# Performance work log

Measured on AMD Instinct MI355X. Metric: run time of the kernel, lower is better.

Reference implementation:

```python
import jax, jax.numpy as jnp
import numpy as np

L, H, HM, E = 2, 1024, 256, 64  # layers, hidden, hyper hidden, hyper embedding
B, T, D = 64, 256, 1024         # batch, time, input size (D == H so layers stack)


def setup_inputs() -> dict:
    key = jax.random.key(0)
    ks = jax.random.split(key, 16)
    n = jax.random.normal
    inp = {
        'x':   n(ks[0], (B, T, D), jnp.float32),
        # main LSTM weights: 4 gates (i,f,g,o); last dim is the input dim
        'Wx':  n(ks[1], (L, 4, H, D), jnp.float32) / np.sqrt(D),
        'Wh':  n(ks[2], (L, 4, H, H), jnp.float32) / np.sqrt(H),
        # hyper (meta) LSTM: input is concat(x_t, h) of size D+H
        'Wmx': n(ks[3], (L, 4 * HM, D + H), jnp.float32) / np.sqrt(D + H),
        'Wmh': n(ks[4], (L, 4 * HM, HM), jnp.float32) / np.sqrt(HM),
        'bm':  jnp.zeros((L, 4 * HM), jnp.float32),
        # hyper embeddings z per gate (hidden->4xE projections)
        'Wzx': n(ks[5], (L, HM, 4, E), jnp.float32) / np.sqrt(HM),
        'bzx': jnp.ones((L, 4, E), jnp.float32),
        'Wzh': n(ks[6], (L, HM, 4, E), jnp.float32) / np.sqrt(HM),
        'bzh': jnp.ones((L, 4, E), jnp.float32),
        'Wzb': n(ks[7], (L, HM, 4, E), jnp.float32) / np.sqrt(HM),
        # embedding -> per-unit modulation (E->H per gate)
        'Px':  n(ks[8], (L, 4, E, H), jnp.float32) / np.sqrt(E),
        'Ph':  n(ks[9], (L, 4, E, H), jnp.float32) / np.sqrt(E),
        'Pb':  n(ks[10], (L, 4, E, H), jnp.float32) / np.sqrt(E),
    }
    return inp


def _meta_lstm_forward(x, Wx, Wh, Wmx, Wmh, bm, Wzx, bzx, Wzh, bzh, Wzb, Px, Ph, Pb):
    Bb = x.shape[0]
    inp = x
    for l in range(L):
        def step(carry, xt, l=l):
            h, c, mh, mc = carry
            # hyper LSTM step on concat(x_t, h)
            xcat = jnp.concatenate([xt, h], axis=-1)
            mpre = xcat @ Wmx[l].T + mh @ Wmh[l].T + bm[l]
            mi, mf, mg, mo = jnp.split(mpre, 4, axis=-1)
            mc2 = jax.nn.sigmoid(mf) * mc + jax.nn.sigmoid(mi) * jnp.tanh(mg)
            mh2 = jax.nn.sigmoid(mo) * jnp.tanh(mc2)
            # gate embeddings and per-unit modulation vectors [B,4,H]
            zx = jnp.einsum('bm,mge->bge', mh2, Wzx[l]) + bzx[l]
            zh = jnp.einsum('bm,mge->bge', mh2, Wzh[l]) + bzh[l]
            zb = jnp.einsum('bm,mge->bge', mh2, Wzb[l])
            dx = jnp.einsum('bge,geh->bgh', zx, Px[l])
            dh = jnp.einsum('bge,geh->bgh', zh, Ph[l])
            db = jnp.einsum('bge,geh->bgh', zb, Pb[l])
            # main LSTM gate pre-activations, hyper-modulated
            gx = jnp.einsum('bd,ghd->bgh', xt, Wx[l])
            gh = jnp.einsum('bk,ghk->bgh', h, Wh[l])
            pre = dx * gx + dh * gh + db
            i_, f_, g_, o_ = pre[:, 0], pre[:, 1], pre[:, 2], pre[:, 3]
            c2 = jax.nn.sigmoid(f_) * c + jax.nn.sigmoid(i_) * jnp.tanh(g_)
            h2 = jax.nn.sigmoid(o_) * jnp.tanh(c2)
            return (h2, c2, mh2, mc2), h2
        init = (jnp.zeros((Bb, H), x.dtype), jnp.zeros((Bb, H), x.dtype),
                jnp.zeros((Bb, HM), x.dtype), jnp.zeros((Bb, HM), x.dtype))
        xs = jnp.swapaxes(inp, 0, 1)  # [T,B,D]
        _, hs = jax.lax.scan(step, init, xs)
        inp = jnp.swapaxes(hs, 0, 1)  # [B,T,H]
    return inp


def reference(x, Wx, Wh, Wmx, Wmh, bm, Wzx, bzx, Wzh, bzh, Wzb, Px, Ph, Pb):
    return _meta_lstm_forward(x, Wx, Wh, Wmx, Wmh, bm, Wzx, bzx, Wzh, bzh, Wzb, Px, Ph, Pb)
```

## Files before the change

### kernel.cpp

```cpp
#include <hip/hip_runtime.h>
#include <hip/hip_cooperative_groups.h>

namespace cg = cooperative_groups;

#define Bb 64
#define Tt 256
#define Dd 1024
#define Hh 1024
#define HMm 256
#define Ee 64

__device__ __forceinline__ float b2f(unsigned short u){
    union{unsigned int i; float f;} v; v.i = ((unsigned int)u) << 16; return v.f;
}
__device__ __forceinline__ unsigned short f2bf(float f){
    union{float f; unsigned int i;} v; v.f = f;
    unsigned int x = v.i;
    unsigned int r = (x + 0x7fffu + ((x >> 16) & 1u)) >> 16;
    return (unsigned short)r;
}
__device__ __forceinline__ void up2(unsigned int u, float& lo, float& hi){
    union{unsigned int i; float f;} x, y;
    x.i = u << 16; y.i = u & 0xffff0000u; lo = x.f; hi = y.f;
}
__device__ __forceinline__ float sigf(float x){ return 1.f/(1.f + expf(-x)); }

__device__ __forceinline__ float ldT(const unsigned short* p){ return b2f(*p); }
__device__ __forceinline__ float ldT(const float* p){ return *p; }
__device__ __forceinline__ void stT(unsigned short* p, float v){ *p = f2bf(v); }
__device__ __forceinline__ void stT(float* p, float v){ *p = v; }

__device__ __forceinline__ void ld8(const unsigned short* p, float* f){
    uint4 u = *(const uint4*)(const void*)p;
    up2(u.x,f[0],f[1]); up2(u.y,f[2],f[3]); up2(u.z,f[4],f[5]); up2(u.w,f[6],f[7]);
}
__device__ __forceinline__ void ld8(const float* p, float* f){
    float4 a = *(const float4*)(const void*)p;
    float4 b = *(const float4*)(const void*)(p+4);
    f[0]=a.x; f[1]=a.y; f[2]=a.z; f[3]=a.w; f[4]=b.x; f[5]=b.y; f[6]=b.z; f[7]=b.w;
}
__device__ __forceinline__ float dot8(const float* a, const float* b, float acc){
    #pragma unroll
    for(int i=0;i<8;i++) acc += a[i]*b[i];
    return acc;
}

__global__ void k_detect(const unsigned short* __restrict__ x, int* __restrict__ flag){
    int tid = threadIdx.x;
    float v = fabsf(b2f(x[2 * tid]));
    bool in = (v > 1e-4f) && (v < 50.f);
    unsigned long long m = __ballot(in);
    if(tid == 0) *flag = (__popcll(m) >= 32) ? 0 : 1;
}

template<typename T>
__global__ __launch_bounds__(1024, 4) void coop_rnn(
    const T* x,
    const T* __restrict__ Wx, const T* __restrict__ Wh,
    const T* __restrict__ Wmx, const T* __restrict__ Wmh, const T* __restrict__ bm,
    const T* __restrict__ Wzx, const T* __restrict__ bzx,
    const T* __restrict__ Wzh, const T* __restrict__ bzh, const T* __restrict__ Wzb,
    const T* __restrict__ Px, const T* __restrict__ Ph, const T* __restrict__ Pb,
    T* out, float* ws, const int* flag)
{
    if(*flag != (int)(sizeof(T) == 4)) return;
    cg::grid_group grid = cg::this_grid();

    float* h0   = ws;
    float* h1   = ws + 65536;
    float* cst  = ws + 131072;
    float* m0   = ws + 196608;
    float* m1   = ws + 212992;
    float* mcst = ws + 229376;
    float* z    = ws + 245760;
    float* xbuf = ws + 294912;

    int tid = threadIdx.x, bid = blockIdx.x;

    __shared__ float sA[256];
    __shared__ float spre[1024];

    for(int l = 0; l < 2; l++){
        const T* xseq = l ? out : x;
        const T* Wx_l  = Wx  + (size_t)l * 4194304;
        const T* Wh_l  = Wh  + (size_t)l * 4194304;
        const T* Wmx_l = Wmx + (size_t)l * 2097152;
        const T* Wmh_l = Wmh + (size_t)l * 262144;
        const T* bm_l  = bm  + l * 1024;
        const T* Wz0 = Wzx + l * 65536;
        const T* Wz1 = Wzh + l * 65536;
        const T* Wz2 = Wzb + l * 65536;
        const T* bz0 = bzx + l * 256;
        const T* bz1 = bzh + l * 256;
        const T* Px_l = Px + l * 262144;
        const T* Ph_l = Ph + l * 262144;
        const T* Pb_l = Pb + l * 262144;

        {
            int gid = bid * 1024 + tid;
            if(gid < 65536){ h0[gid] = 0.f; cst[gid] = 0.f; }
            if(gid < 16384){ m0[gid] = 0.f; mcst[gid] = 0.f; }
        }
        float *hp = h0, *hn = h1, *mp = m0, *mn = m1;
        grid.sync();

        for(int t = 0; t < 256; t++){
            {
                int sg = bid * 1024 + tid;
                if(sg < 65536){
                    int xb = sg >> 10, xd = sg & 1023;
                    xbuf[sg] = ldT(&xseq[((size_t)xb * Tt + t) * Dd + xd]);
                }

                int r  = tid >> 8;
                int b  = (tid >> 2) & 63;
                int ks = tid & 3;
                int row = r * 256 + bid;
                const T* wr = Wmx_l + (size_t)row * 2048;
                const T* wm = Wmh_l + (size_t)row * 256;
                const T* xr = xseq + ((size_t)b * Tt + t) * Dd;
                const float* hr = hp + b * 1024;
                const float* mr = mp + b * 256;
                float a0 = 0.f, a1 = 0.f, a2 = 0.f, a3 = 0.f;
                float wf[8], vf[8];
                int k0 = ks * 256;
                for(int k = k0; k < k0 + 256; k += 16){
                    ld8(wr + k, wf);      ld8(xr + k, vf);      a0 = dot8(wf, vf, a0);
                    ld8(wr + k + 8, wf);  ld8(xr + k + 8, vf);  a1 = dot8(wf, vf, a1);
                }
                for(int k = k0; k < k0 + 256; k += 16){
                    ld8(wr + 1024 + k, wf);     ld8(hr + k, vf);     a2 = dot8(wf, vf, a2);
                    ld8(wr + 1024 + k + 8, wf); ld8(hr + k + 8, vf); a3 = dot8(wf, vf, a3);
                }
                int ms = ks * 64;
                for(int m = ms; m < ms + 64; m += 16){
                    ld8(wm + m, wf);     ld8(mr + m, vf);     a0 = dot8(wf, vf, a0);
                    ld8(wm + m + 8, wf); ld8(mr + m + 8, vf); a1 = dot8(wf, vf, a1);
                }
                float a = (a0 + a1) + (a2 + a3);
                a += __shfl_xor(a, 1);
                a += __shfl_xor(a, 2);
                if(ks == 0) sA[r * 64 + b] = a + ldT(&bm_l[row]);
            }
            __syncthreads();
            if(tid < 64){
                int b = tid;
                float mi = sA[b], mf = sA[64 + b], mg = sA[128 + b], mo = sA[192 + b];
                int idx = b * 256 + bid;
                float mc2 = sigf(mf) * mcst[idx] + sigf(mi) * tanhf(mg);
                mcst[idx] = mc2;
                mn[idx] = sigf(mo) * tanhf(mc2);
            }
            grid.sync();

            if(bid < 192){
                int s_ = bid >> 6, b = bid & 63;
                int ks = tid >> 8, col = tid & 255;
                const T* W = (s_ == 0) ? Wz0 : ((s_ == 1) ? Wz1 : Wz2);
                const float* mr = mn + b * 256;
                float acc = 0.f;
                int ms = ks * 64;
                #pragma unroll 8
                for(int m = ms; m < ms + 64; m++)
                    acc += mr[m] * ldT(&W[m * 256 + col]);
                spre[tid] = acc;
                __syncthreads();
                if(tid < 256){
                    float biasv = (s_ == 0) ? ldT(&bz0[tid]) : ((s_ == 1) ? ldT(&bz1[tid]) : 0.f);
                    z[(s_ * 64 + b) * 256 + tid] =
                        biasv + ((spre[tid] + spre[256 + tid]) + (spre[512 + tid] + spre[768 + tid]));
                }
            }
            grid.sync();

            {
                int r16 = tid >> 6;
                int g = r16 >> 2, hh = r16 & 3;
                int bg = (tid >> 2) & 15;
                int ks = tid & 3;
                int h = bid * 4 + hh;
                int n = g * 1024 + h;
                int b0 = bg * 4;
                const T* wxr = Wx_l + (size_t)n * 1024;
                const T* whr = Wh_l + (size_t)n * 1024;
                float gx[4] = {0,0,0,0}, gh[4] = {0,0,0,0};
                int k0 = ks * 256;
                for(int k = k0; k < k0 + 256; k += 8){
                    float wf[8]; ld8(wxr + k, wf);
                    #pragma unroll
                    for(int i = 0; i < 4; i++){
                        float xf[8]; ld8(xbuf + (b0 + i) * 1024 + k, xf);
                        gx[i] = dot8(wf, xf, gx[i]);
                    }
                }
                for(int k = k0; k < k0 + 256; k += 8){
                    float wf[8]; ld8(whr + k, wf);
                    #pragma unroll
                    for(int i = 0; i < 4; i++){
                        float hf[8]; ld8(hp + (b0 + i) * 1024 + k, hf);
                        gh[i] = dot8(wf, hf, gh[i]);
                    }
                }
                float dx[4] = {0,0,0,0}, dh[4] = {0,0,0,0}, db[4] = {0,0,0,0};
                int e0 = ks * 16;
                for(int e = e0; e < e0 + 16; e++){
                    int pi = (g * 64 + e) * 1024 + h;
                    float pxv = ldT(&Px_l[pi]);
                    float phv = ldT(&Ph_l[pi]);
                    float pbv = ldT(&Pb_l[pi]);
                    int zc = g * 64 + e;
                    #pragma unroll
                    for(int i = 0; i < 4; i++){
                        int b = b0 + i;
                        dx[i] += z[(b) * 256 + zc] * pxv;
                        dh[i] += z[(64 + b) * 256 + zc] * phv;
                        db[i] += z[(128 + b) * 256 + zc] * pbv;
                    }
                }
                #pragma unroll
                for(int i = 0; i < 4; i++){
                    gx[i] += __shfl_xor(gx[i], 1); gx[i] += __shfl_xor(gx[i], 2);
                    gh[i] += __shfl_xor(gh[i], 1); gh[i] += __shfl_xor(gh[i], 2);
                    dx[i] += __shfl_xor(dx[i], 1); dx[i] += __shfl_xor(dx[i], 2);
                    dh[i] += __shfl_xor(dh[i], 1); dh[i] += __shfl_xor(dh[i], 2);
                    db[i] += __shfl_xor(db[i], 1); db[i] += __shfl_xor(db[i], 2);
                }
                if(ks == 0){
                    #pragma unroll
                    for(int i = 0; i < 4; i++)
                        spre[r16 * 64 + b0 + i] = dx[i] * gx[i] + dh[i] * gh[i] + db[i];
                }
            }
            __syncthreads();
            if(tid < 256){
                int hh = tid >> 6, b = tid & 63;
                float pi_ = spre[(0 * 4 + hh) * 64 + b];
                float pf_ = spre[(1 * 4 + hh) * 64 + b];
                float pg_ = spre[(2 * 4 + hh) * 64 + b];
                float po_ = spre[(3 * 4 + hh) * 64 + b];
                int h = bid * 4 + hh;
                int idx = b * 1024 + h;
                float c2 = sigf(pf_) * cst[idx] + sigf(pi_) * tanhf(pg_);
                float h2 = sigf(po_) * tanhf(c2);
                cst[idx] = c2;
                hn[idx] = h2;
                stT(&out[((size_t)b * Tt + t) * Dd + h], h2);
            }
            grid.sync();

            float* tp = hp; hp = hn; hn = tp;
            tp = mp; mp = mn; mn = tp;
        }
    }
}

template<typename T>
static void launch_path(void* const* d_in, void* d_out, float* ws, int* flag, hipStream_t stream){
    const T* xp   = (const T*)d_in[0];
    const T* Wxp  = (const T*)d_in[1];
    const T* Whp  = (const T*)d_in[2];
    const T* Wmxp = (const T*)d_in[3];
    const T* Wmhp = (const T*)d_in[4];
    const T* bmp  = (const T*)d_in[5];
    const T* Wzxp = (const T*)d_in[6];
    const T* bzxp = (const T*)d_in[7];
    const T* Wzhp = (const T*)d_in[8];
    const T* bzhp = (const T*)d_in[9];
    const T* Wzbp = (const T*)d_in[10];
    const T* Pxp  = (const T*)d_in[11];
    const T* Php  = (const T*)d_in[12];
    const T* Pbp  = (const T*)d_in[13];
    T* outp = (T*)d_out;
    void* args[] = {
        (void*)&xp, (void*)&Wxp, (void*)&Whp, (void*)&Wmxp, (void*)&Wmhp, (void*)&bmp,
        (void*)&Wzxp, (void*)&bzxp, (void*)&Wzhp, (void*)&bzhp, (void*)&Wzbp,
        (void*)&Pxp, (void*)&Php, (void*)&Pbp, (void*)&outp, (void*)&ws, (void*)&flag
    };
    hipLaunchCooperativeKernel((void*)coop_rnn<T>, dim3(256), dim3(1024), args, 0, stream);
}

extern "C" void kernel_launch(void* const* d_in, const int* in_sizes, int n_in,
                              void* d_out, int out_size, void* d_ws, size_t ws_size,
                              hipStream_t stream) {
    (void)in_sizes; (void)n_in; (void)out_size; (void)ws_size;
    float* ws = (float*)d_ws;
    int* flag = (int*)(ws + 360448);

    k_detect<<<1, 64, 0, stream>>>((const unsigned short*)d_in[0], flag);
    launch_path<unsigned short>(d_in, d_out, ws, flag, stream);
    launch_path<float>(d_in, d_out, ws, flag, stream);
}
```

Measured before the change: 288.1 ms.

## Keep per-block weight slices resident in LDS for bf16 cooperative RNN

Splits the templated kernel into separate bf16 and f32 kernels. The bf16 kernel loads each block's slices of Wx, Wh, Wmx, Wmh, Wz and P into shared memory once per layer instead of re-reading them from global memory every timestep. It also distributes the z-embedding projection across all blocks with a transposed z layout that allows vectorized float4 reads, and stores the staged x as bf16. This uses roughly 85KB of LDS per block, which limits occupancy and relies on the large LDS capacity; the f32 path is left unchanged.

```diff
diff --git a/kernel.cpp b/kernel.cpp
--- a/kernel.cpp
+++ b/kernel.cpp
@@ -53,17 +53,19 @@
     if(tid == 0) *flag = (__popcll(m) >= 32) ? 0 : 1;
 }
 
-template<typename T>
-__global__ __launch_bounds__(1024, 4) void coop_rnn(
-    const T* x,
-    const T* __restrict__ Wx, const T* __restrict__ Wh,
-    const T* __restrict__ Wmx, const T* __restrict__ Wmh, const T* __restrict__ bm,
-    const T* __restrict__ Wzx, const T* __restrict__ bzx,
-    const T* __restrict__ Wzh, const T* __restrict__ bzh, const T* __restrict__ Wzb,
-    const T* __restrict__ Px, const T* __restrict__ Ph, const T* __restrict__ Pb,
-    T* out, float* ws, const int* flag)
+__global__ __launch_bounds__(1024, 4) void coop_rnn_bf16(
+    const unsigned short* x,
+    const unsigned short* __restrict__ Wx, const unsigned short* __restrict__ Wh,
+    const unsigned short* __restrict__ Wmx, const unsigned short* __restrict__ Wmh,
+    const unsigned short* __restrict__ bm,
+    const unsigned short* __restrict__ Wzx, const unsigned short* __restrict__ bzx,
+    const unsigned short* __restrict__ Wzh, const unsigned short* __restrict__ bzh,
+    const unsigned short* __restrict__ Wzb,
+    const unsigned short* __restrict__ Px, const unsigned short* __restrict__ Ph,
+    const unsigned short* __restrict__ Pb,
+    unsigned short* out, float* ws, const int* flag)
 {
-    if(*flag != (int)(sizeof(T) == 4)) return;
+    if(*flag != 0) return;
     cg::grid_group grid = cg::this_grid();
 
     float* h0   = ws;
@@ -73,34 +75,81 @@
     float* m1   = ws + 212992;
     float* mcst = ws + 229376;
     float* z    = ws + 245760;
-    float* xbuf = ws + 294912;
+    unsigned short* xbuf16 = (unsigned short*)(ws + 294912);
 
     int tid = threadIdx.x, bid = blockIdx.x;
 
+    __shared__ __align__(16) unsigned short sWx[16][4][264];
+    __shared__ __align__(16) unsigned short sWh[16][4][264];
+    __shared__ __align__(16) unsigned short sWmxX[4][4][264];
+    __shared__ __align__(16) unsigned short sWmxH[4][4][264];
+    __shared__ __align__(16) unsigned short sWmh[4][4][72];
+    __shared__ __align__(16) unsigned short sWz[3][4][72];
+    __shared__ __align__(16) unsigned short sP[3][4][64][4];
+    __shared__ float sBm[4], sBz[2];
     __shared__ float sA[256];
     __shared__ float spre[1024];
 
     for(int l = 0; l < 2; l++){
-        const T* xseq = l ? out : x;
-        const T* Wx_l  = Wx  + (size_t)l * 4194304;
-        const T* Wh_l  = Wh  + (size_t)l * 4194304;
-        const T* Wmx_l = Wmx + (size_t)l * 2097152;
-        const T* Wmh_l = Wmh + (size_t)l * 262144;
-        const T* bm_l  = bm  + l * 1024;
-        const T* Wz0 = Wzx + l * 65536;
-        const T* Wz1 = Wzh + l * 65536;
-        const T* Wz2 = Wzb + l * 65536;
-        const T* bz0 = bzx + l * 256;
-        const T* bz1 = bzh + l * 256;
-        const T* Px_l = Px + l * 262144;
-        const T* Ph_l = Ph + l * 262144;
-        const T* Pb_l = Pb + l * 262144;
+        const unsigned short* xseq = l ? out : x;
+        const unsigned short* Wx_l  = Wx  + (size_t)l * 4194304;
+        const unsigned short* Wh_l  = Wh  + (size_t)l * 4194304;
+        const unsigned short* Wmx_l = Wmx + (size_t)l * 2097152;
+        const unsigned short* Wmh_l = Wmh + (size_t)l * 262144;
+        const unsigned short* bm_l  = bm  + l * 1024;
+        const unsigned short* Wz0 = Wzx + l * 65536;
+        const unsigned short* Wz1 = Wzh + l * 65536;
+        const unsigned short* Wz2 = Wzb + l * 65536;
+        const unsigned short* bz0 = bzx + l * 256;
+        const unsigned short* bz1 = bzh + l * 256;
+        const unsigned short* Px_l = Px + l * 262144;
+        const unsigned short* Ph_l = Ph + l * 262144;
+        const unsigned short* Pb_l = Pb + l * 262144;
 
         {
             int gid = bid * 1024 + tid;
             if(gid < 65536){ h0[gid] = 0.f; cst[gid] = 0.f; }
             if(gid < 16384){ m0[gid] = 0.f; mcst[gid] = 0.f; }
         }
+
+        for(int idx = tid; idx < 16384; idx += 1024){
+            int rr = idx >> 10, k = idx & 1023;
+            int g = rr >> 2, hh = rr & 3;
+            size_t n = (size_t)(g * 1024 + bid * 4 + hh);
+            sWx[rr][k >> 8][k & 255] = Wx_l[n * 1024 + k];
+        }
+        for(int idx = tid; idx < 16384; idx += 1024){
+            int rr = idx >> 10, k = idx & 1023;
+            int g = rr >> 2, hh = rr & 3;
+            size_t n = (size_t)(g * 1024 + bid * 4 + hh);
+            sWh[rr][k >> 8][k & 255] = Wh_l[n * 1024 + k];
+        }
+        for(int idx = tid; idx < 4096; idx += 1024){
+            int r = idx >> 10, k = idx & 1023;
+            size_t row = (size_t)(r * 256 + bid);
+            sWmxX[r][k >> 8][k & 255] = Wmx_l[row * 2048 + k];
+            sWmxH[r][k >> 8][k & 255] = Wmx_l[row * 2048 + 1024 + k];
+        }
+        {
+            int r = tid >> 8, m = tid & 255;
+            sWmh[r][m >> 6][m & 63] = Wmh_l[(size_t)(r * 256 + bid) * 256 + m];
+        }
+        if(tid < 768){
+            int s_ = tid >> 8, m = tid & 255;
+            const unsigned short* W = (s_ == 0) ? Wz0 : ((s_ == 1) ? Wz1 : Wz2);
+            sWz[s_][m >> 6][m & 63] = W[m * 256 + bid];
+        }
+        {
+            int g = tid >> 8, e = (tid >> 2) & 63, hh = tid & 3;
+            int pi = (g * 64 + e) * 1024 + bid * 4 + hh;
+            sP[0][g][e][hh] = Px_l[pi];
+            sP[1][g][e][hh] = Ph_l[pi];
+            sP[2][g][e][hh] = Pb_l[pi];
+        }
+        if(tid < 4) sBm[tid] = ldT(&bm_l[tid * 256 + bid]);
+        if(tid == 4) sBz[0] = ldT(&bz0[bid]);
+        if(tid == 5) sBz[1] = ldT(&bz1[bid]);
+
         float *hp = h0, *hn = h1, *mp = m0, *mn = m1;
         grid.sync();
 
@@ -109,38 +158,36 @@
                 int sg = bid * 1024 + tid;
                 if(sg < 65536){
                     int xb = sg >> 10, xd = sg & 1023;
-                    xbuf[sg] = ldT(&xseq[((size_t)xb * Tt + t) * Dd + xd]);
+                    xbuf16[sg] = xseq[((size_t)xb * Tt + t) * Dd + xd];
                 }
 
                 int r  = tid >> 8;
                 int b  = (tid >> 2) & 63;
                 int ks = tid & 3;
-                int row = r * 256 + bid;
-                const T* wr = Wmx_l + (size_t)row * 2048;
-                const T* wm = Wmh_l + (size_t)row * 256;
-                const T* xr = xseq + ((size_t)b * Tt + t) * Dd;
-                const float* hr = hp + b * 1024;
-                const float* mr = mp + b * 256;
+                const unsigned short* wxp = &sWmxX[r][ks][0];
+                const unsigned short* whp_ = &sWmxH[r][ks][0];
+                const unsigned short* wmp = &sWmh[r][ks][0];
+                const unsigned short* xr = xseq + ((size_t)b * Tt + t) * Dd + ks * 256;
+                const float* hr = hp + b * 1024 + ks * 256;
+                const float* mr = mp + b * 256 + ks * 64;
                 float a0 = 0.f, a1 = 0.f, a2 = 0.f, a3 = 0.f;
                 float wf[8], vf[8];
-                int k0 = ks * 256;
-                for(int k = k0; k < k0 + 256; k += 16){
-                    ld8(wr + k, wf);      ld8(xr + k, vf);      a0 = dot8(wf, vf, a0);
-                    ld8(wr + k + 8, wf);  ld8(xr + k + 8, vf);  a1 = dot8(wf, vf, a1);
-                }
-                for(int k = k0; k < k0 + 256; k += 16){
-                    ld8(wr + 1024 + k, wf);     ld8(hr + k, vf);     a2 = dot8(wf, vf, a2);
-                    ld8(wr + 1024 + k + 8, wf); ld8(hr + k + 8, vf); a3 = dot8(wf, vf, a3);
-                }
-                int ms = ks * 64;
-                for(int m = ms; m < ms + 64; m += 16){
-                    ld8(wm + m, wf);     ld8(mr + m, vf);     a0 = dot8(wf, vf, a0);
-                    ld8(wm + m + 8, wf); ld8(mr + m + 8, vf); a1 = dot8(wf, vf, a1);
+                for(int k = 0; k < 256; k += 16){
+                    ld8(wxp + k, wf);     ld8(xr + k, vf);     a0 = dot8(wf, vf, a0);
+                    ld8(wxp + k + 8, wf); ld8(xr + k + 8, vf); a1 = dot8(wf, vf, a1);
+                }
+                for(int k = 0; k < 256; k += 16){
+                    ld8(whp_ + k, wf);     ld8(hr + k, vf);     a2 = dot8(wf, vf, a2);
+                    ld8(whp_ + k + 8, wf); ld8(hr + k + 8, vf); a3 = dot8(wf, vf, a3);
+                }
+                for(int m = 0; m < 64; m += 16){
+                    ld8(wmp + m, wf);     ld8(mr + m, vf);     a0 = dot8(wf, vf, a0);
+                    ld8(wmp + m + 8, wf); ld8(mr + m + 8, vf); a1 = dot8(wf, vf, a1);
                 }
                 float a = (a0 + a1) + (a2 + a3);
                 a += __shfl_xor(a, 1);
                 a += __shfl_xor(a, 2);
-                if(ks == 0) sA[r * 64 + b] = a + ldT(&bm_l[row]);
+                if(ks == 0) sA[r * 64 + b] = a + sBm[r];
             }
             __syncthreads();
             if(tid < 64){
@@ -153,22 +200,21 @@
             }
             grid.sync();
 
-            if(bid < 192){
-                int s_ = bid >> 6, b = bid & 63;
-                int ks = tid >> 8, col = tid & 255;
-                const T* W = (s_ == 0) ? Wz0 : ((s_ == 1) ? Wz1 : Wz2);
-                const float* mr = mn + b * 256;
-                float acc = 0.f;
-                int ms = ks * 64;
-                #pragma unroll 8
-                for(int m = ms; m < ms + 64; m++)
-                    acc += mr[m] * ldT(&W[m * 256 + col]);
-                spre[tid] = acc;
-                __syncthreads();
-                if(tid < 256){
-                    float biasv = (s_ == 0) ? ldT(&bz0[tid]) : ((s_ == 1) ? ldT(&bz1[tid]) : 0.f);
-                    z[(s_ * 64 + b) * 256 + tid] =
-                        biasv + ((spre[tid] + spre[256 + tid]) + (spre[512 + tid] + spre[768 + tid]));
+            if(tid < 768){
+                int s_ = tid >> 8, sub = tid & 255;
+                int b = sub >> 2, ks = sub & 3;
+                const unsigned short* wz = &sWz[s_][ks][0];
+                const float* mr = mn + b * 256 + ks * 64;
+                float acc = 0.f; float wf[8], vf[8];
+                for(int m = 0; m < 64; m += 16){
+                    ld8(wz + m, wf);     ld8(mr + m, vf);     acc = dot8(wf, vf, acc);
+                    ld8(wz + m + 8, wf); ld8(mr + m + 8, vf); acc = dot8(wf, vf, acc);
+                }
+                acc += __shfl_xor(acc, 1);
+                acc += __shfl_xor(acc, 2);
+                if(ks == 0){
+                    float biasv = (s_ == 0) ? sBz[0] : ((s_ == 1) ? sBz[1] : 0.f);
+                    z[((s_ * 256) + bid) * 64 + b] = acc + biasv;
                 }
             }
             grid.sync();
@@ -178,44 +224,39 @@
                 int g = r16 >> 2, hh = r16 & 3;
                 int bg = (tid >> 2) & 15;
                 int ks = tid & 3;
-                int h = bid * 4 + hh;
-                int n = g * 1024 + h;
                 int b0 = bg * 4;
-                const T* wxr = Wx_l + (size_t)n * 1024;
-                const T* whr = Wh_l + (size_t)n * 1024;
+                const unsigned short* wxr = &sWx[r16][ks][0];
+                const unsigned short* whr = &sWh[r16][ks][0];
                 float gx[4] = {0,0,0,0}, gh[4] = {0,0,0,0};
-                int k0 = ks * 256;
-                for(int k = k0; k < k0 + 256; k += 8){
+                for(int k = 0; k < 256; k += 8){
                     float wf[8]; ld8(wxr + k, wf);
                     #pragma unroll
                     for(int i = 0; i < 4; i++){
-                        float xf[8]; ld8(xbuf + (b0 + i) * 1024 + k, xf);
+                        float xf[8]; ld8(xbuf16 + (b0 + i) * 1024 + ks * 256 + k, xf);
                         gx[i] = dot8(wf, xf, gx[i]);
                     }
                 }
-                for(int k = k0; k < k0 + 256; k += 8){
+                for(int k = 0; k < 256; k += 8){
                     float wf[8]; ld8(whr + k, wf);
                     #pragma unroll
                     for(int i = 0; i < 4; i++){
-                        float hf[8]; ld8(hp + (b0 + i) * 1024 + k, hf);
+                        float hf[8]; ld8(hp + (b0 + i) * 1024 + ks * 256 + k, hf);
                         gh[i] = dot8(wf, hf, gh[i]);
                     }
                 }
                 float dx[4] = {0,0,0,0}, dh[4] = {0,0,0,0}, db[4] = {0,0,0,0};
                 int e0 = ks * 16;
                 for(int e = e0; e < e0 + 16; e++){
-                    int pi = (g * 64 + e) * 1024 + h;
-                    float pxv = ldT(&Px_l[pi]);
-                    float phv = ldT(&Ph_l[pi]);
-                    float pbv = ldT(&Pb_l[pi]);
                     int zc = g * 64 + e;
-                    #pragma unroll
-                    for(int i = 0; i < 4; i++){
-                        int b = b0 + i;
-                        dx[i] += z[(b) * 256 + zc] * pxv;
-                        dh[i] += z[(64 + b) * 256 + zc] * phv;
-                        db[i] += z[(128 + b) * 256 + zc] * pbv;
-                    }
+                    float pxv = b2f(sP[0][g][e][hh]);
+                    float phv = b2f(sP[1][g][e][hh]);
+                    float pbv = b2f(sP[2][g][e][hh]);
+                    const float4 zx4 = *(const float4*)&z[(0 * 256 + zc) * 64 + b0];
+                    const float4 zh4 = *(const float4*)&z[(1 * 256 + zc) * 64 + b0];
+                    const float4 zb4 = *(const float4*)&z[(2 * 256 + zc) * 64 + b0];
+                    dx[0] += zx4.x * pxv; dx[1] += zx4.y * pxv; dx[2] += zx4.z * pxv; dx[3] += zx4.w * pxv;
+                    dh[0] += zh4.x * phv; dh[1] += zh4.y * phv; dh[2] += zh4.z * phv; dh[3] += zh4.w * phv;
+                    db[0] += zb4.x * pbv; db[1] += zb4.y * pbv; db[2] += zb4.z * pbv; db[3] += zb4.w * pbv;
                 }
                 #pragma unroll
                 for(int i = 0; i < 4; i++){
@@ -254,29 +295,251 @@
     }
 }
 
-template<typename T>
-static void launch_path(void* const* d_in, void* d_out, float* ws, int* flag, hipStream_t stream){
-    const T* xp   = (const T*)d_in[0];
-    const T* Wxp  = (const T*)d_in[1];
-    const T* Whp  = (const T*)d_in[2];
-    const T* Wmxp = (const T*)d_in[3];
-    const T* Wmhp = (const T*)d_in[4];
-    const T* bmp  = (const T*)d_in[5];
-    const T* Wzxp = (const T*)d_in[6];
-    const T* bzxp = (const T*)d_in[7];
-    const T* Wzhp = (const T*)d_in[8];
-    const T* bzhp = (const T*)d_in[9];
-    const T* Wzbp = (const T*)d_in[10];
-    const T* Pxp  = (const T*)d_in[11];
-    const T* Php  = (const T*)d_in[12];
-    const T* Pbp  = (const T*)d_in[13];
-    T* outp = (T*)d_out;
+__global__ __launch_bounds__(1024, 4) void coop_rnn_f32(
+    const float* x,
+    const float* __restrict__ Wx, const float* __restrict__ Wh,
+    const float* __restrict__ Wmx, const float* __restrict__ Wmh, const float* __restrict__ bm,
+    const float* __restrict__ Wzx, const float* __restrict__ bzx,
+    const float* __restrict__ Wzh, const float* __restrict__ bzh, const float* __restrict__ Wzb,
+    const float* __restrict__ Px, const float* __restrict__ Ph, const float* __restrict__ Pb,
+    float* out, float* ws, const int* flag)
+{
+    if(*flag != 1) return;
+    cg::grid_group grid = cg::this_grid();
+
+    float* h0   = ws;
+    float* h1   = ws + 65536;
+    float* cst  = ws + 131072;
+    float* m0   = ws + 196608;
+    float* m1   = ws + 212992;
+    float* mcst = ws + 229376;
+    float* z    = ws + 245760;
+    float* xbuf = ws + 294912;
+
+    int tid = threadIdx.x, bid = blockIdx.x;
+
+    __shared__ float sA[256];
+    __shared__ float spre[1024];
+
+    for(int l = 0; l < 2; l++){
+        const float* xseq = l ? out : x;
+        const float* Wx_l  = Wx  + (size_t)l * 4194304;
+        const float* Wh_l  = Wh  + (size_t)l * 4194304;
+        const float* Wmx_l = Wmx + (size_t)l * 2097152;
+        const float* Wmh_l = Wmh + (size_t)l * 262144;
+        const float* bm_l  = bm  + l * 1024;
+        const float* Wz0 = Wzx + l * 65536;
+        const float* Wz1 = Wzh + l * 65536;
+        const float* Wz2 = Wzb + l * 65536;
+        const float* bz0 = bzx + l * 256;
+        const float* bz1 = bzh + l * 256;
+        const float* Px_l = Px + l * 262144;
+        const float* Ph_l = Ph + l * 262144;
+        const float* Pb_l = Pb + l * 262144;
+
+        {
+            int gid = bid * 1024 + tid;
+            if(gid < 65536){ h0[gid] = 0.f; cst[gid] = 0.f; }
+            if(gid < 16384){ m0[gid] = 0.f; mcst[gid] = 0.f; }
+        }
+        float *hp = h0, *hn = h1, *mp = m0, *mn = m1;
+        grid.sync();
+
+        for(int t = 0; t < 256; t++){
+            {
+                int sg = bid * 1024 + tid;
+                if(sg < 65536){
+                    int xb = sg >> 10, xd = sg & 1023;
+                    xbuf[sg] = ldT(&xseq[((size_t)xb * Tt + t) * Dd + xd]);
+                }
+                int r  = tid >> 8;
+                int b  = (tid >> 2) & 63;
+                int ks = tid & 3;
+                int row = r * 256 + bid;
+                const float* wr = Wmx_l + (size_t)row * 2048;
+                const float* wm = Wmh_l + (size_t)row * 256;
+                const float* xr = xseq + ((size_t)b * Tt + t) * Dd;
+                const float* hr = hp + b * 1024;
+                const float* mr = mp + b * 256;
+                float a0 = 0.f, a1 = 0.f, a2 = 0.f, a3 = 0.f;
+                float wf[8], vf[8];
+                int k0 = ks * 256;
+                for(int k = k0; k < k0 + 256; k += 16){
+                    ld8(wr + k, wf);      ld8(xr + k, vf);      a0 = dot8(wf, vf, a0);
+                    ld8(wr + k + 8, wf);  ld8(xr + k + 8, vf);  a1 = dot8(wf, vf, a1);
+                }
+                for(int k = k0; k < k0 + 256; k += 16){
+                    ld8(wr + 1024 + k, wf);     ld8(hr + k, vf);     a2 = dot8(wf, vf, a2);
+                    ld8(wr + 1024 + k + 8, wf); ld8(hr + k + 8, vf); a3 = dot8(wf, vf, a3);
+                }
+                int ms = ks * 64;
+                for(int m = ms; m < ms + 64; m += 16){
+                    ld8(wm + m, wf);     ld8(mr + m, vf);     a0 = dot8(wf, vf, a0);
+                    ld8(wm + m + 8, wf); ld8(mr + m + 8, vf); a1 = dot8(wf, vf, a1);
+                }
+                float a = (a0 + a1) + (a2 + a3);
+                a += __shfl_xor(a, 1);
+                a += __shfl_xor(a, 2);
+                if(ks == 0) sA[r * 64 + b] = a + ldT(&bm_l[row]);
+            }
+            __syncthreads();
+            if(tid < 64){
+                int b = tid;
+                float mi = sA[b], mf = sA[64 + b], mg = sA[128 + b], mo = sA[192 + b];
+                int idx = b * 256 + bid;
+                float mc2 = sigf(mf) * mcst[idx] + sigf(mi) * tanhf(mg);
+                mcst[idx] = mc2;
+                mn[idx] = sigf(mo) * tanhf(mc2);
+            }
+            grid.sync();
+
+            if(bid < 192){
+                int s_ = bid >> 6, b = bid & 63;
+                int ks = tid >> 8, col = tid & 255;
+                const float* W = (s_ == 0) ? Wz0 : ((s_ == 1) ? Wz1 : Wz2);
+                const float* mr = mn + b * 256;
+                float acc = 0.f;
+                int ms = ks * 64;
+                #pragma unroll 8
+                for(int m = ms; m < ms + 64; m++)
+                    acc += mr[m] * ldT(&W[m * 256 + col]);
+                spre[tid] = acc;
+                __syncthreads();
+                if(tid < 256){
+                    float biasv = (s_ == 0) ? ldT(&bz0[tid]) : ((s_ == 1) ? ldT(&bz1[tid]) : 0.f);
+                    z[(s_ * 64 + b) * 256 + tid] =
+                        biasv + ((spre[tid] + spre[256 + tid]) + (spre[512 + tid] + spre[768 + tid]));
+                }
+            }
+            grid.sync();
+
+            {
+                int r16 = tid >> 6;
+                int g = r16 >> 2, hh = r16 & 3;
+                int bg = (tid >> 2) & 15;
+                int ks = tid & 3;
+                int h = bid * 4 + hh;
+                int n = g * 1024 + h;
+                int b0 = bg * 4;
+                const float* wxr = Wx_l + (size_t)n * 1024;
+                const float* whr = Wh_l + (size_t)n * 1024;
+                float gx[4] = {0,0,0,0}, gh[4] = {0,0,0,0};
+                int k0 = ks * 256;
+                for(int k = k0; k < k0 + 256; k += 8){
+                    float wf[8]; ld8(wxr + k, wf);
+                    #pragma unroll
+                    for(int i = 0; i < 4; i++){
+                        float xf[8]; ld8(xbuf + (b0 + i) * 1024 + k, xf);
+                        gx[i] = dot8(wf, xf, gx[i]);
+                    }
+                }
+                for(int k = k0; k < k0 + 256; k += 8){
+                    float wf[8]; ld8(whr + k, wf);
+                    #pragma unroll
+                    for(int i = 0; i < 4; i++){
+                        float hf[8]; ld8(hp + (b0 + i) * 1024 + k, hf);
+                        gh[i] = dot8(wf, hf, gh[i]);
+                    }
+                }
+                float dx[4] = {0,0,0,0}, dh[4] = {0,0,0,0}, db[4] = {0,0,0,0};
+                int e0 = ks * 16;
+                for(int e = e0; e < e0 + 16; e++){
+                    int pi = (g * 64 + e) * 1024 + h;
+                    float pxv = ldT(&Px_l[pi]);
+                    float phv = ldT(&Ph_l[pi]);
+                    float pbv = ldT(&Pb_l[pi]);
+                    int zc = g * 64 + e;
+                    #pragma unroll
+                    for(int i = 0; i < 4; i++){
+                        int b = b0 + i;
+                        dx[i] += z[(b) * 256 + zc] * pxv;
+                        dh[i] += z[(64 + b) * 256 + zc] * phv;
+                        db[i] += z[(128 + b) * 256 + zc] * pbv;
+                    }
+                }
+                #pragma unroll
+                for(int i = 0; i < 4; i++){
+                    gx[i] += __shfl_xor(gx[i], 1); gx[i] += __shfl_xor(gx[i], 2);
+                    gh[i] += __shfl_xor(gh[i], 1); gh[i] += __shfl_xor(gh[i], 2);
+                    dx[i] += __shfl_xor(dx[i], 1); dx[i] += __shfl_xor(dx[i], 2);
+                    dh[i] += __shfl_xor(dh[i], 1); dh[i] += __shfl_xor(dh[i], 2);
+                    db[i] += __shfl_xor(db[i], 1); db[i] += __shfl_xor(db[i], 2);
+                }
+                if(ks == 0){
+                    #pragma unroll
+                    for(int i = 0; i < 4; i++)
+                        spre[r16 * 64 + b0 + i] = dx[i] * gx[i] + dh[i] * gh[i] + db[i];
+                }
+            }
+            __syncthreads();
+            if(tid < 256){
+                int hh = tid >> 6, b = tid & 63;
+                float pi_ = spre[(0 * 4 + hh) * 64 + b];
+                float pf_ = spre[(1 * 4 + hh) * 64 + b];
+                float pg_ = spre[(2 * 4 + hh) * 64 + b];
+                float po_ = spre[(3 * 4 + hh) * 64 + b];
+                int h = bid * 4 + hh;
+                int idx = b * 1024 + h;
+                float c2 = sigf(pf_) * cst[idx] + sigf(pi_) * tanhf(pg_);
+                float h2 = sigf(po_) * tanhf(c2);
+                cst[idx] = c2;
+                hn[idx] = h2;
+                stT(&out[((size_t)b * Tt + t) * Dd + h], h2);
+            }
+            grid.sync();
+
+            float* tp = hp; hp = hn; hn = tp;
+            tp = mp; mp = mn; mn = tp;
+        }
+    }
+}
+
+static void launch_bf16(void* const* d_in, void* d_out, float* ws, int* flag, hipStream_t stream){
+    const unsigned short* xp   = (const unsigned short*)d_in[0];
+    const unsigned short* Wxp  = (const unsigned short*)d_in[1];
+    const unsigned short* Whp  = (const unsigned short*)d_in[2];
+    const unsigned short* Wmxp = (const unsigned short*)d_in[3];
+    const unsigned short* Wmhp = (const unsigned short*)d_in[4];
+    const unsigned short* bmp  = (const unsigned short*)d_in[5];
+    const unsigned short* Wzxp = (const unsigned short*)d_in[6];
+    const unsigned short* bzxp = (const unsigned short*)d_in[7];
+    const unsigned short* Wzhp = (const unsigned short*)d_in[8];
+    const unsigned short* bzhp = (const unsigned short*)d_in[9];
+    const unsigned short* Wzbp = (const unsigned short*)d_in[10];
+    const unsigned short* Pxp  = (const unsigned short*)d_in[11];
+    const unsigned short* Php  = (const unsigned short*)d_in[12];
+    const unsigned short* Pbp  = (const unsigned short*)d_in[13];
+    unsigned short* outp = (unsigned short*)d_out;
     void* args[] = {
         (void*)&xp, (void*)&Wxp, (void*)&Whp, (void*)&Wmxp, (void*)&Wmhp, (void*)&bmp,
         (void*)&Wzxp, (void*)&bzxp, (void*)&Wzhp, (void*)&bzhp, (void*)&Wzbp,
         (void*)&Pxp, (void*)&Php, (void*)&Pbp, (void*)&outp, (void*)&ws, (void*)&flag
     };
-    hipLaunchCooperativeKernel((void*)coop_rnn<T>, dim3(256), dim3(1024), args, 0, stream);
+    hipLaunchCooperativeKernel((void*)coop_rnn_bf16, dim3(256), dim3(1024), args, 0, stream);
+}
+
+static void launch_f32(void* const* d_in, void* d_out, float* ws, int* flag, hipStream_t stream){
+    const float* xp   = (const float*)d_in[0];
+    const float* Wxp  = (const float*)d_in[1];
+    const float* Whp  = (const float*)d_in[2];
+    const float* Wmxp = (const float*)d_in[3];
+    const float* Wmhp = (const float*)d_in[4];
+    const float* bmp  = (const float*)d_in[5];
+    const float* Wzxp = (const float*)d_in[6];
+    const float* bzxp = (const float*)d_in[7];
+    const float* Wzhp = (const float*)d_in[8];
+    const float* bzhp = (const float*)d_in[9];
+    const float* Wzbp = (const float*)d_in[10];
+    const float* Pxp  = (const float*)d_in[11];
+    const float* Php  = (const float*)d_in[12];
+    const float* Pbp  = (const float*)d_in[13];
+    float* outp = (float*)d_out;
+    void* args[] = {
+        (void*)&xp, (void*)&Wxp, (void*)&Whp, (void*)&Wmxp, (void*)&Wmhp, (void*)&bmp,
+        (void*)&Wzxp, (void*)&bzxp, (void*)&Wzhp, (void*)&bzhp, (void*)&Wzbp,
+        (void*)&Pxp, (void*)&Php, (void*)&Pbp, (void*)&outp, (void*)&ws, (void*)&flag
+    };
+    hipLaunchCooperativeKernel((void*)coop_rnn_f32, dim3(256), dim3(1024), args, 0, stream);
 }
 
 extern "C" void kernel_launch(void* const* d_in, const int* in_sizes, int n_in,
@@ -287,6 +550,6 @@
     int* flag = (int*)(ws + 360448);
 
     k_detect<<<1, 64, 0, stream>>>((const unsigned short*)d_in[0], flag);
-    launch_path<unsigned short>(d_in, d_out, ws, flag, stream);
-    launch_path<float>(d_in, d_out, ws, flag, stream);
-}
+    launch_bf16(d_in, d_out, ws, flag, stream);
+    launch_f32(d_in, d_out, ws, flag, stream);
+}
```

Result: no change. 287.7 ms (-0.1%).
